# Optimization experiments

Measured on AMD Instinct MI355X. Metric: run time of the kernel, lower is better.

## Reference

```python
import jax, jax.numpy as jnp
import numpy as np

B, T, D = 64, 512, 41  # batch, target timesteps, channels (input_dim)


def setup_inputs() -> dict:
    key = jax.random.key(0)
    k1, k2, k3 = jax.random.split(key, 3)
    target_x = jax.random.uniform(k1, (B, T), dtype=jnp.float32)
    vals = jax.random.normal(k2, (B, T, D), dtype=jnp.float32)
    mask = jax.random.randint(k3, (B, T, D), 0, 2, dtype=jnp.int32)
    return {"target_x": target_x, "vals": vals, "mask": mask}


def reference(target_x, vals, mask):
    # Faithful vectorized version of TRIPLETFORMER.compute_unsupervised_loss's
    # ragged target assembly (the torch code loops over the batch with boolean
    # indexing + F.pad; here we left-pack with a stable argsort on the mask).
    b, t, d = vals.shape
    L = t * d  # full_len = tau.size(1) * self.dim

    tau = jnp.broadcast_to(target_x[:, :, None], (b, t, d)).reshape(b, L)
    U = vals.reshape(b, L)
    mk = mask.reshape(b, L)
    # C = cumsum(ones, -1) - 1 over channel axis == arange(d) broadcast
    C = jnp.broadcast_to(jnp.arange(d, dtype=jnp.int32), (b, t, d)).reshape(b, L)

    # Stable sort: observed entries (mk==1) packed to the front, order preserved.
    order = jnp.argsort(1 - mk, axis=-1, stable=True)  # [B, L]
    take = lambda x: jnp.take_along_axis(x, order, axis=-1)

    mk_p = take(mk)                                   # sorted mask: 1s then 0s
    valid = mk_p.astype(tau.dtype)
    tau_p = take(tau) * valid                         # pad with 0, as F.pad(value=0)
    U_p = take(U) * valid
    C_p = take(C) * mk_p                              # padded C entries -> 0 (matches torch pad)

    C_onehot = jax.nn.one_hot(C_p, d, dtype=tau.dtype)            # [B, L, D]
    target_context = jnp.concatenate([tau_p[:, :, None], C_onehot], -1)  # [B, L, 1+D]
    # target_mask = stack([C_, mk], -1); target_vals = U packed.
    # (The data-dependent obs_len truncation in torch is a pure slice of zero
    #  rows; omitted here to keep static shapes — values are identical.)
    out = jnp.concatenate(
        [target_context,                # [:, :, :1+D]  tau + one-hot channel
         U_p[:, :, None],               # packed target values
         valid[:, :, None]],            # packed observation mask
        axis=-1)                        # [B, L, D+3]
    return out
```

## Files before the change

### kernel.cpp

```cpp
#include <hip/hip_runtime.h>

#define BB 64
#define TT 512
#define DD 41
#define LL (TT * DD)
#define COLS (DD + 3)
#define NTH 1024
#define CHUNK ((LL + NTH - 1) / NTH)

__global__ __launch_bounds__(NTH)
void tf_scan_kernel(const int* __restrict__ mask, int* __restrict__ srcIdx) {
    const int b   = blockIdx.x;
    const int tid = threadIdx.x;
    const int* mrow = mask + (size_t)b * LL;
    int* srow = srcIdx + (size_t)b * LL;

    const int begin = tid * CHUNK;

    int mloc[CHUNK];
    int cnt = 0;
#pragma unroll
    for (int i = 0; i < CHUNK; ++i) {
        const int l = begin + i;
        const int m = (l < LL) ? mrow[l] : 0;
        mloc[i] = m;
        cnt += m;
    }

    __shared__ int s[NTH];
    s[tid] = cnt;
    __syncthreads();
    for (int off = 1; off < NTH; off <<= 1) {
        const int v = (tid >= off) ? s[tid - off] : 0;
        __syncthreads();
        s[tid] += v;
        __syncthreads();
    }
    const int nObs = s[NTH - 1];
    int eObs = s[tid] - cnt;

#pragma unroll
    for (int i = 0; i < CHUNK; ++i) {
        const int l = begin + i;
        if (l >= LL) break;
        if (mloc[i]) {
            srow[eObs] = l + 1;
            ++eObs;
        } else {
            srow[nObs + (l - eObs)] = -(l + 1);
        }
    }
}

__global__ __launch_bounds__(256)
void tf_emit_kernel(const float* __restrict__ target_x,
                    const float* __restrict__ vals,
                    const int* __restrict__ srcIdx,
                    float* __restrict__ out,
                    int total4) {
    const int o = blockIdx.x * blockDim.x + threadIdx.x;
    if (o >= total4) return;

    const int c4 = o % 11;
    const int pg = o / 11;
    const int b  = pg / LL;

    const int raw   = srcIdx[pg];
    const bool valid = raw > 0;
    const int l  = (valid ? raw : -raw) - 1;
    const int t  = l / DD;
    const int ch = valid ? (l - t * DD) : 0;
    const float vm  = valid ? 1.0f : 0.0f;
    const float tau = target_x[b * TT + t] * vm;
    const float U   = vals[(size_t)b * LL + l] * vm;

    const int c0 = c4 * 4;
    float v[4];
#pragma unroll
    for (int j = 0; j < 4; ++j) {
        const int c = c0 + j;
        float x;
        if (c == 0)            x = tau;
        else if (c <= DD)      x = (c - 1 == ch) ? 1.0f : 0.0f;
        else if (c == DD + 1)  x = U;
        else                   x = vm;
        v[j] = x;
    }
    float4 r;
    r.x = v[0]; r.y = v[1]; r.z = v[2]; r.w = v[3];
    reinterpret_cast<float4*>(out)[o] = r;
}

extern "C" void kernel_launch(void* const* d_in, const int* in_sizes, int n_in,
                              void* d_out, int out_size, void* d_ws, size_t ws_size,
                              hipStream_t stream) {
    const float* target_x = (const float*)d_in[0];
    const float* vals     = (const float*)d_in[1];
    const int*   mask     = (const int*)d_in[2];
    float* out = (float*)d_out;
    int* srcIdx = (int*)d_ws;

    tf_scan_kernel<<<BB, NTH, 0, stream>>>(mask, srcIdx);

    const int total4 = BB * LL * (COLS / 4);
    const int blocks = (total4 + 255) / 256;
    tf_emit_kernel<<<blocks, 256, 0, stream>>>(target_x, vals, srcIdx, out, total4);
}
```

Measured before the change: 281.1 us.

## Tile emit kernel by rows, stage per-row gather in LDS, nontemporal stores

The emit kernel now assigns each 256-thread block a tile of 256 packed rows. Each thread does that row's srcIdx, target_x and vals gather exactly once and stores the results in shared memory. The block then writes the 11 float4 chunks of every row cooperatively from LDS using nontemporal stores. This removes the 11x redundant per-row gathers and index divisions of the old one-thread-per-float4 scheme, and keeps the large write-only output from polluting the cache, at the cost of one barrier per block.

```diff
diff --git a/kernel.cpp b/kernel.cpp
--- a/kernel.cpp
+++ b/kernel.cpp
@@ -5,8 +5,14 @@
 #define DD 41
 #define LL (TT * DD)
 #define COLS (DD + 3)
+#define F4_PER_ROW (COLS / 4)
 #define NTH 1024
 #define CHUNK ((LL + NTH - 1) / NTH)
+
+#define ROWS 256
+#define TILES_PER_B (LL / ROWS)
+
+typedef float f4v __attribute__((ext_vector_type(4)));
 
 __global__ __launch_bounds__(NTH)
 void tf_scan_kernel(const int* __restrict__ mask, int* __restrict__ srcIdx) {
@@ -52,43 +58,56 @@
     }
 }
 
-__global__ __launch_bounds__(256)
+__global__ __launch_bounds__(ROWS)
 void tf_emit_kernel(const float* __restrict__ target_x,
                     const float* __restrict__ vals,
                     const int* __restrict__ srcIdx,
-                    float* __restrict__ out,
-                    int total4) {
-    const int o = blockIdx.x * blockDim.x + threadIdx.x;
-    if (o >= total4) return;
+                    float* __restrict__ out) {
+    __shared__ f4v info[ROWS];
 
-    const int c4 = o % 11;
-    const int pg = o / 11;
-    const int b  = pg / LL;
+    const int blk  = blockIdx.x;
+    const int b    = blk / TILES_PER_B;
+    const int tile = blk - b * TILES_PER_B;
+    const int pg0  = b * LL + tile * ROWS;
 
-    const int raw   = srcIdx[pg];
-    const bool valid = raw > 0;
-    const int l  = (valid ? raw : -raw) - 1;
-    const int t  = l / DD;
-    const int ch = valid ? (l - t * DD) : 0;
-    const float vm  = valid ? 1.0f : 0.0f;
-    const float tau = target_x[b * TT + t] * vm;
-    const float U   = vals[(size_t)b * LL + l] * vm;
+    {
+        const int r   = threadIdx.x;
+        const int raw = srcIdx[pg0 + r];
+        const bool valid = raw > 0;
+        const int l  = (valid ? raw : -raw) - 1;
+        const int t  = l / DD;
+        const int ch = valid ? (l - t * DD) : 0;
+        const float vm  = valid ? 1.0f : 0.0f;
+        const float tau = target_x[b * TT + t] * vm;
+        const float U   = vals[(size_t)b * LL + l] * vm;
+        f4v inf;
+        inf.x = tau; inf.y = U; inf.z = __int_as_float(ch); inf.w = vm;
+        info[r] = inf;
+    }
+    __syncthreads();
 
-    const int c0 = c4 * 4;
-    float v[4];
+    f4v* outp = reinterpret_cast<f4v*>(out) + (size_t)pg0 * F4_PER_ROW;
 #pragma unroll
-    for (int j = 0; j < 4; ++j) {
-        const int c = c0 + j;
-        float x;
-        if (c == 0)            x = tau;
-        else if (c <= DD)      x = (c - 1 == ch) ? 1.0f : 0.0f;
-        else if (c == DD + 1)  x = U;
-        else                   x = vm;
-        v[j] = x;
+    for (int k = 0; k < F4_PER_ROW; ++k) {
+        const int q  = k * ROWS + threadIdx.x;
+        const int rr = q / F4_PER_ROW;
+        const int c4 = q - rr * F4_PER_ROW;
+        const f4v inf = info[rr];
+        const int ch = __float_as_int(inf.z);
+        const int c0 = c4 * 4;
+        f4v rv;
+#pragma unroll
+        for (int j = 0; j < 4; ++j) {
+            const int c = c0 + j;
+            float x;
+            if (c == 0)            x = inf.x;
+            else if (c <= DD)      x = (c - 1 == ch) ? 1.0f : 0.0f;
+            else if (c == DD + 1)  x = inf.y;
+            else                   x = inf.w;
+            rv[j] = x;
+        }
+        __builtin_nontemporal_store(rv, &outp[q]);
     }
-    float4 r;
-    r.x = v[0]; r.y = v[1]; r.z = v[2]; r.w = v[3];
-    reinterpret_cast<float4*>(out)[o] = r;
 }
 
 extern "C" void kernel_launch(void* const* d_in, const int* in_sizes, int n_in,
@@ -102,7 +121,6 @@
 
     tf_scan_kernel<<<BB, NTH, 0, stream>>>(mask, srcIdx);
 
-    const int total4 = BB * LL * (COLS / 4);
-    const int blocks = (total4 + 255) / 256;
-    tf_emit_kernel<<<blocks, 256, 0, stream>>>(target_x, vals, srcIdx, out, total4);
+    const int blocks = BB * TILES_PER_B;
+    tf_emit_kernel<<<blocks, ROWS, 0, stream>>>(target_x, vals, srcIdx, out);
 }
```

Result: faster. 268.6 us (-4.5%).

## Replace per-batch scan with tiled three-pass count/scan/emit using wave ballots

Applied to the files above, without the earlier changes.

The old path used one 1024-thread block per batch row for the stream compaction, then a separate emit pass that gathered through a scattered index array. The new code counts observed entries per 256-element tile with wave ballots and scans the tile counts per batch. Each tile then compacts locally in shared memory and writes its output rows directly. This spreads the scan across many blocks instead of 64 and removes the srcIdx round trip and the gather. The cost is an extra small kernel launch and a second read of the mask.

```diff
diff --git a/kernel.cpp b/kernel.cpp
--- a/kernel.cpp
+++ b/kernel.cpp
@@ -5,90 +5,111 @@
 #define DD 41
 #define LL (TT * DD)
 #define COLS (DD + 3)
-#define NTH 1024
-#define CHUNK ((LL + NTH - 1) / NTH)
+#define F4R (COLS / 4)
+#define TILE 256
+#define TPB (LL / TILE)
+#define NTILES (BB * TPB)
 
-__global__ __launch_bounds__(NTH)
-void tf_scan_kernel(const int* __restrict__ mask, int* __restrict__ srcIdx) {
+typedef float f4v __attribute__((ext_vector_type(4)));
+
+
+__global__ __launch_bounds__(TILE)
+void k1_count(const int* __restrict__ mask, int* __restrict__ partials) {
+    const int blk = blockIdx.x;
+    const int tid = threadIdx.x;
+    const int m = mask[(size_t)blk * TILE + tid];
+    const unsigned long long bal = __ballot(m != 0);
+    __shared__ int ws[4];
+    if ((tid & 63) == 0) ws[tid >> 6] = __popcll(bal);
+    __syncthreads();
+    if (tid == 0) partials[blk] = ws[0] + ws[1] + ws[2] + ws[3];
+}
+
+__global__ __launch_bounds__(128)
+void k2_scan(const int* __restrict__ partials, int* __restrict__ tileOff,
+             int* __restrict__ nObs) {
     const int b   = blockIdx.x;
     const int tid = threadIdx.x;
-    const int* mrow = mask + (size_t)b * LL;
-    int* srow = srcIdx + (size_t)b * LL;
-
-    const int begin = tid * CHUNK;
-
-    int mloc[CHUNK];
-    int cnt = 0;
-#pragma unroll
-    for (int i = 0; i < CHUNK; ++i) {
-        const int l = begin + i;
-        const int m = (l < LL) ? mrow[l] : 0;
-        mloc[i] = m;
-        cnt += m;
-    }
-
-    __shared__ int s[NTH];
-    s[tid] = cnt;
+    const int v = (tid < TPB) ? partials[b * TPB + tid] : 0;
+    __shared__ int s[128];
+    s[tid] = v;
     __syncthreads();
-    for (int off = 1; off < NTH; off <<= 1) {
-        const int v = (tid >= off) ? s[tid - off] : 0;
+    for (int off = 1; off < 128; off <<= 1) {
+        const int t = (tid >= off) ? s[tid - off] : 0;
         __syncthreads();
-        s[tid] += v;
+        s[tid] += t;
         __syncthreads();
     }
-    const int nObs = s[NTH - 1];
-    int eObs = s[tid] - cnt;
-
-#pragma unroll
-    for (int i = 0; i < CHUNK; ++i) {
-        const int l = begin + i;
-        if (l >= LL) break;
-        if (mloc[i]) {
-            srow[eObs] = l + 1;
-            ++eObs;
-        } else {
-            srow[nObs + (l - eObs)] = -(l + 1);
-        }
-    }
+    if (tid < TPB) tileOff[b * TPB + tid] = s[tid] - v;
+    if (tid == TPB - 1) nObs[b] = s[tid];
 }
 
-__global__ __launch_bounds__(256)
-void tf_emit_kernel(const float* __restrict__ target_x,
-                    const float* __restrict__ vals,
-                    const int* __restrict__ srcIdx,
-                    float* __restrict__ out,
-                    int total4) {
-    const int o = blockIdx.x * blockDim.x + threadIdx.x;
-    if (o >= total4) return;
+__global__ __launch_bounds__(TILE)
+void k3_emit(const float* __restrict__ target_x, const float* __restrict__ vals,
+             const int* __restrict__ mask, const int* __restrict__ tileOff,
+             const int* __restrict__ nObs, float* __restrict__ out) {
+    const int blk = blockIdx.x;
+    const int tid = threadIdx.x;
+    const int b     = blk / TPB;
+    const int lrow0 = (blk - b * TPB) * TILE;
+    const size_t src = (size_t)blk * TILE + tid;
 
-    const int c4 = o % 11;
-    const int pg = o / 11;
-    const int b  = pg / LL;
+    const int   m    = mask[src] != 0;
+    const float Uraw = vals[src];
+    const int lrow = lrow0 + tid;
+    const int t  = lrow / DD;
+    const int ch = lrow - t * DD;
+    const float tau = target_x[b * TT + t];
 
-    const int raw   = srcIdx[pg];
-    const bool valid = raw > 0;
-    const int l  = (valid ? raw : -raw) - 1;
-    const int t  = l / DD;
-    const int ch = valid ? (l - t * DD) : 0;
-    const float vm  = valid ? 1.0f : 0.0f;
-    const float tau = target_x[b * TT + t] * vm;
-    const float U   = vals[(size_t)b * LL + l] * vm;
+    const unsigned long long bal = __ballot(m);
+    const int lane = tid & 63;
+    const int w    = tid >> 6;
+    const int rankInWave = __popcll(bal & ((1ull << lane) - 1ull));
+    __shared__ int wsum[4];
+    if (lane == 0) wsum[w] = __popcll(bal);
+    __syncthreads();
+    const int s0 = wsum[0], s1 = wsum[1], s2 = wsum[2], s3 = wsum[3];
+    const int cntObs = s0 + s1 + s2 + s3;
+    const int wbase  = (w > 0 ? s0 : 0) + (w > 1 ? s1 : 0) + (w > 2 ? s2 : 0);
+    const int eObs = wbase + rankInWave;
+    const int d = m ? eObs : cntObs + (tid - eObs);
 
-    const int c0 = c4 * 4;
-    float v[4];
+    __shared__ f4v info[TILE];
+    f4v inf;
+    inf.x = m ? tau : 0.0f;
+    inf.y = m ? Uraw : 0.0f;
+    inf.z = __int_as_float(m ? ch : 0);
+    inf.w = m ? 1.0f : 0.0f;
+    info[d] = inf;
+    __syncthreads();
+
+    const int tOff    = tileOff[blk];
+    const int padRow0 = nObs[b] + (lrow0 - tOff);
+    const size_t rowBase = (size_t)b * LL;
+
+    f4v* outp = reinterpret_cast<f4v*>(out);
 #pragma unroll
-    for (int j = 0; j < 4; ++j) {
-        const int c = c0 + j;
-        float x;
-        if (c == 0)            x = tau;
-        else if (c <= DD)      x = (c - 1 == ch) ? 1.0f : 0.0f;
-        else if (c == DD + 1)  x = U;
-        else                   x = vm;
-        v[j] = x;
+    for (int k = 0; k < F4R; ++k) {
+        const int q  = k * TILE + tid;
+        const int rr = q / F4R;
+        const int c4 = q - rr * F4R;
+        const f4v v = info[rr];
+        const int chh = __float_as_int(v.z);
+        const int gr = (rr < cntObs) ? (tOff + rr) : (padRow0 + (rr - cntObs));
+        const int c0 = c4 * 4;
+        f4v rv;
+#pragma unroll
+        for (int j = 0; j < 4; ++j) {
+            const int c = c0 + j;
+            float x;
+            if (c == 0)            x = v.x;
+            else if (c <= DD)      x = (c - 1 == chh) ? 1.0f : 0.0f;
+            else if (c == DD + 1)  x = v.y;
+            else                   x = v.w;
+            rv[j] = x;
+        }
+        outp[(rowBase + (size_t)gr) * F4R + c4] = rv;
     }
-    float4 r;
-    r.x = v[0]; r.y = v[1]; r.z = v[2]; r.w = v[3];
-    reinterpret_cast<float4*>(out)[o] = r;
 }
 
 extern "C" void kernel_launch(void* const* d_in, const int* in_sizes, int n_in,
@@ -98,11 +119,12 @@
     const float* vals     = (const float*)d_in[1];
     const int*   mask     = (const int*)d_in[2];
     float* out = (float*)d_out;
-    int* srcIdx = (int*)d_ws;
 
-    tf_scan_kernel<<<BB, NTH, 0, stream>>>(mask, srcIdx);
+    int* partials = (int*)d_ws;
+    int* tileOff  = partials + NTILES;
+    int* nObs     = tileOff + NTILES;
 
-    const int total4 = BB * LL * (COLS / 4);
-    const int blocks = (total4 + 255) / 256;
-    tf_emit_kernel<<<blocks, 256, 0, stream>>>(target_x, vals, srcIdx, out, total4);
+    k1_count<<<NTILES, TILE, 0, stream>>>(mask, partials);
+    k2_scan<<<BB, 128, 0, stream>>>(partials, tileOff, nObs);
+    k3_emit<<<NTILES, TILE, 0, stream>>>(target_x, vals, mask, tileOff, nObs, out);
 }
```

After: 247.4 us. 12.0% less time.
